# Kernel tuning notes

Hardware: AMD Instinct MI355X
Metric: run time of the kernel (lower is better)

The kernel has to match this reference:

```python
import jax, jax.numpy as jnp
import numpy as np

EPS = 1e-8

def _rasterize_mesh(face_verts, H, W):
    # face_verts: [F,3,3] = (ndc_x, ndc_y, view_z) per triangle vertex
    x0, y0, z0 = face_verts[:, 0, 0], face_verts[:, 0, 1], face_verts[:, 0, 2]
    x1, y1, z1 = face_verts[:, 1, 0], face_verts[:, 1, 1], face_verts[:, 1, 2]
    x2, y2, z2 = face_verts[:, 2, 0], face_verts[:, 2, 1], face_verts[:, 2, 2]
    area = (x1 - x0) * (y2 - y0) - (y1 - y0) * (x2 - x0)
    # cull_backfaces=True (area<=0) + degenerate + behind-camera cull
    face_ok = (area > EPS) & (z0 > 0) & (z1 > 0) & (z2 > 0)
    inv_area = jnp.where(face_ok, 1.0 / jnp.where(face_ok, area, 1.0), 0.0)
    zs = jnp.stack([z0, z1, z2], -1)  # [F,3]
    # pytorch3d NDC: +x left, +y up, pixel centers
    xs = 1.0 - (2.0 * jnp.arange(W, dtype=jnp.float32) + 1.0) / W
    ys = 1.0 - (2.0 * jnp.arange(H, dtype=jnp.float32) + 1.0) / H

    def row_fn(py):
        px = xs[:, None]  # [W,1] broadcast vs faces [F]
        w0 = ((x1 - px) * (y2 - py) - (y1 - py) * (x2 - px)) * inv_area
        w1 = ((x2 - px) * (y0 - py) - (y2 - py) * (x0 - px)) * inv_area
        w2 = ((x0 - px) * (y1 - py) - (y0 - py) * (x1 - px)) * inv_area
        inside = (w0 >= 0) & (w1 >= 0) & (w2 >= 0) & face_ok
        # perspective_correct=True: l_i = w_i * prod(other z), renormalize
        l = jnp.stack([w0 * z1 * z2, z0 * w1 * z2, z0 * z1 * w2], -1)  # [W,F,3]
        s = l.sum(-1, keepdims=True)
        b = l / jnp.where(s == 0, 1.0, s)
        # clip_barycentric_coords=True
        b = jnp.clip(b, 0.0, None)
        b = b / jnp.clip(b.sum(-1, keepdims=True), EPS, None)
        zpix = (b * zs[None]).sum(-1)  # [W,F] interpolated view-space depth
        zm = jnp.where(inside, zpix, jnp.inf)
        fidx = jnp.argmin(zm, axis=1)  # z-buffer winner per pixel
        zmin = jnp.take_along_axis(zm, fidx[:, None], 1)[:, 0]
        hit = jnp.isfinite(zmin)
        bary = jnp.take_along_axis(b, fidx[:, None, None], 1)[:, 0]  # [W,3]
        return (jnp.where(hit, fidx, -1),
                jnp.where(hit, zmin, -1.0),
                jnp.where(hit[:, None], bary, -1.0))

    return jax.lax.map(row_fn, ys)  # ([H,W],[H,W],[H,W,3])


def _forward(positions, features, faces, K, RT, H, W):
    B, V, _ = positions.shape
    Fn = faces.shape[1]
    # --- create_camera_objects: open3d/opencv KRT -> pytorch3d camera ---
    R = RT[:, :, :3]
    t = RT[:, :, 3]
    scale = min(H, W) / 2.0
    focal = jnp.stack([K[:, 0, 0], K[:, 1, 1]], -1) / scale  # [B,2] NDC focal
    p0 = -(jnp.stack([K[:, 0, 2], K[:, 1, 2]], -1)
           - jnp.array([W / 2.0, H / 2.0], jnp.float32)) / scale  # [B,2]
    sign = jnp.array([-1.0, -1.0, 1.0], jnp.float32)
    R_p = jnp.swapaxes(R, 1, 2) * sign[None, None, :]  # R^T with cols 0,1 negated
    T_p = t * sign[None, :]
    # --- _get_mesh_ndc: world -> view -> NDC (pytorch3d row-vector convention) ---
    v_view = jnp.einsum('bvi,bij->bvj', positions, R_p) + T_p[:, None, :]
    z = v_view[..., 2:3]
    xy_ndc = focal[:, None, :] * v_view[..., :2] / z + p0[:, None, :]
    verts_ndc = jnp.concatenate([xy_ndc, z], -1)  # z overwritten with view-space depth
    face_verts = jax.vmap(lambda v, f: v[f])(verts_ndc, faces)  # [B,F,3,3]
    # --- rasterize (blur_sigma=0 -> faces_per_pixel=1) ---
    p2f, zbuf, bary = jax.vmap(lambda fv: _rasterize_mesh(fv, H, W))(face_verts)
    hit = p2f >= 0
    pix_to_face = jnp.where(hit, p2f + (jnp.arange(B) * Fn)[:, None, None], -1)
    # --- interpolate_face_attributes on packed faces/verts ---
    faces_packed = (faces + (jnp.arange(B) * V)[:, None, None]).reshape(B * Fn, 3)
    feats_packed = features.reshape(B * V, -1)
    fv_idx = faces_packed[jnp.clip(pix_to_face, 0)]  # [B,H,W,3]
    attrs = feats_packed[fv_idx]                      # [B,H,W,3,C]
    pix_feats = (bary[..., None] * attrs).sum(-2)
    pix_feats = jnp.where(hit[..., None], pix_feats, 0.0)
    dists = jnp.where(hit, 0.0, -1.0)
    # add faces_per_pixel (K=1) axis, matching pytorch3d Fragments layout
    return (pix_feats[:, :, :, None, :], pix_to_face[:, :, :, None],
            zbuf[:, :, :, None], bary[:, :, :, None, :], dists[:, :, :, None])


def setup_inputs() -> dict:
    key = jax.random.key(0)
    k1, k2, k3 = jax.random.split(key, 3)
    B, V, Fn, C, H, W = 1, 8192, 16384, 64, 192, 192
    positions = jax.random.uniform(k1, (B, V, 3), jnp.float32) * 2.0 - 1.0
    features = jax.random.normal(k2, (B, V, C), jnp.float32)
    faces = jax.random.randint(k3, (B, Fn, 3), 0, V)
    K = jnp.broadcast_to(jnp.array([[180.0, 0.0, 96.0], [0.0, 180.0, 96.0],
                                    [0.0, 0.0, 1.0]], jnp.float32), (B, 3, 3))
    RT = jnp.broadcast_to(jnp.concatenate(
        [jnp.eye(3, dtype=jnp.float32),
         jnp.array([[0.0], [0.0], [3.5]], jnp.float32)], axis=1), (B, 3, 4))
    return {"positions": positions, "features": features, "faces": faces,
            "K": K, "RT": RT, "H": H, "W": W, "blur_sigma": 0}


def reference(positions, features, faces, K, RT, H, W, blur_sigma):
    # blur_sigma == 0 path of VertexShader.forward (faces_per_pixel=1)
    return _forward(positions, features, faces, K, RT, H, W)
```

## Files before the change

kernel.cpp:

```cpp
#include <hip/hip_runtime.h>
#include <stdint.h>

#define H_ 192
#define W_ 192
#define C_ 64
#define EPS_F 1e-8f
#define TILE 16
#define CHUNK 256
#define NSLICE 16

typedef unsigned long long ull;

#define OFF_FEATS 0
#define OFF_P2F   (H_*W_*C_)
#define OFF_ZBUF  (OFF_P2F + H_*W_)
#define OFF_BARY  (OFF_ZBUF + H_*W_)
#define OFF_DIST  (OFF_BARY + H_*W_*3)

__device__ __forceinline__ float xm(float a, float b){ return __fmul_rn(a,b); }
__device__ __forceinline__ float xa(float a, float b){ return __fadd_rn(a,b); }
__device__ __forceinline__ float xsb(float a, float b){ return __fsub_rn(a,b); }
__device__ __forceinline__ float xd(float a, float b){ return __fdiv_rn(a,b); }

__device__ __forceinline__ float pixcoord(int i, float dim){
    float t = xa(xm(2.0f, (float)i), 1.0f);
    return xsb(1.0f, xd(t, dim));
}

__global__ void k_init(const float* __restrict__ pos, const float* __restrict__ K,
                       const float* __restrict__ RT, float* __restrict__ verts,
                       ull* __restrict__ keys, int V){
    int i = blockIdx.x*blockDim.x + threadIdx.x;
    if (i < H_*W_) keys[i] = 0xFFFFFFFFFFFFFFFFULL;
    if (i >= V) return;
    float p0 = pos[3*i+0], p1 = pos[3*i+1], p2 = pos[3*i+2];
    const float sgn[3] = {-1.f, -1.f, 1.f};
    float vv[3];
    #pragma unroll
    for (int j=0;j<3;j++){
        float rp0 = xm(RT[j*4+0], sgn[j]);
        float rp1 = xm(RT[j*4+1], sgn[j]);
        float rp2 = xm(RT[j*4+2], sgn[j]);
        float s = xa(xa(xm(p0,rp0), xm(p1,rp1)), xm(p2,rp2));
        vv[j] = xa(s, xm(RT[j*4+3], sgn[j]));
    }
    float z = vv[2];
    const float scale = 96.0f;
    float fx = xd(K[0], scale);
    float fy = xd(K[4], scale);
    float p0x = -xd(xsb(K[2], 96.0f), scale);
    float p0y = -xd(xsb(K[5], 96.0f), scale);
    float xn = xa(xd(xm(fx, vv[0]), z), p0x);
    float yn = xa(xd(xm(fy, vv[1]), z), p0y);
    verts[4*i+0] = xn; verts[4*i+1] = yn; verts[4*i+2] = z; verts[4*i+3] = 0.f;
}

__global__ void k_faces(const int* __restrict__ faces, const float* __restrict__ verts,
                        float* __restrict__ rec, int Fn){
    int f = blockIdx.x*blockDim.x + threadIdx.x;
    if (f >= Fn) return;
    int i0 = faces[3*f+0], i1 = faces[3*f+1], i2 = faces[3*f+2];
    float x0=verts[4*i0+0], y0=verts[4*i0+1], z0=verts[4*i0+2];
    float x1=verts[4*i1+0], y1=verts[4*i1+1], z1=verts[4*i1+2];
    float x2=verts[4*i2+0], y2=verts[4*i2+1], z2=verts[4*i2+2];
    float area = xsb(xm(xsb(x1,x0), xsb(y2,y0)), xm(xsb(y1,y0), xsb(x2,x0)));
    bool ok = (area > EPS_F) && (z0 > 0.f) && (z1 > 0.f) && (z2 > 0.f);
    float inv_area = ok ? xd(1.0f, area) : 0.0f;
    float xmn, xmx, ymn, ymx, zmn;
    if (ok){
        xmn = fminf(x0, fminf(x1, x2)) - 1e-4f;
        xmx = fmaxf(x0, fmaxf(x1, x2)) + 1e-4f;
        ymn = fminf(y0, fminf(y1, y2)) - 1e-4f;
        ymx = fmaxf(y0, fmaxf(y1, y2)) + 1e-4f;
        zmn = fminf(z0, fminf(z1, z2));
    } else {
        xmn = INFINITY; xmx = -INFINITY; ymn = INFINITY; ymx = -INFINITY;
        zmn = INFINITY;
    }
    float4* q = (float4*)(rec + (size_t)f*16);
    q[0] = make_float4(x0, y0, x1, y1);
    q[1] = make_float4(x2, y2, z0, z1);
    q[2] = make_float4(z2, inv_area, zmn, 0.f);
    q[3] = make_float4(xmn, xmx, ymn, ymx);
}

__global__ __launch_bounds__(256) void k_raster(const float* __restrict__ rec,
        ull* __restrict__ keys, int Fn){
    __shared__ float lds[CHUNK*12];
    __shared__ float zl[CHUNK];
    __shared__ int   slist[CHUNK];
    __shared__ int   wcnt[4];
    int tid = threadIdx.x;
    int ix = blockIdx.x*TILE + (tid & 15);
    int iy = blockIdx.y*TILE + (tid >> 4);
    int pix = iy*W_ + ix;
    float px = pixcoord(ix, (float)W_);
    float py = pixcoord(iy, (float)H_);
    float tx_hi = pixcoord(blockIdx.x*TILE,          (float)W_);
    float tx_lo = pixcoord(blockIdx.x*TILE + TILE-1, (float)W_);
    float ty_hi = pixcoord(blockIdx.y*TILE,          (float)H_);
    float ty_lo = pixcoord(blockIdx.y*TILE + TILE-1, (float)H_);
    int perSlice = Fn / NSLICE;
    int f0 = blockIdx.z * perSlice;
    int f1 = f0 + perSlice;
    int lane = tid & 63, wv = tid >> 6;

    float zbest = INFINITY;
    int fbest = -1;

    for (int base = f0; base < f1; base += CHUNK){
        __syncthreads();
        const float4* g = (const float4*)(rec + (size_t)(base + tid)*16);
        float4 q0 = g[0], q1 = g[1], q2 = g[2], q3 = g[3];
        bool keep = (q3.x <= tx_hi) && (q3.y >= tx_lo) && (q3.z <= ty_hi) && (q3.w >= ty_lo);
        float4* l = (float4*)(lds + tid*12);
        l[0] = q0; l[1] = q1; l[2] = q2;
        ull m = __ballot(keep);
        if (lane == 0) wcnt[wv] = __popcll(m);
        __syncthreads();
        int basecnt = 0;
        #pragma unroll
        for (int w2 = 0; w2 < 4; ++w2) if (w2 < wv) basecnt += wcnt[w2];
        if (keep){
            int pos = basecnt + __popcll(m & ((1ULL << lane) - 1ULL));
            slist[pos] = tid;
            zl[pos] = q2.z;
        }
        int nsurv = wcnt[0] + wcnt[1] + wcnt[2] + wcnt[3];
        __syncthreads();

        for (int k = 0; k < nsurv; k++){
            float zminf = zl[k];
            if (!(xm(zminf, 0.999f) < zbest)) continue;
            int j = slist[k];
            const float* r = lds + j*12;
            float x0=r[0], y0=r[1], x1=r[2], y1=r[3], x2=r[4], y2=r[5];
            float dx0=xsb(x0,px), dx1=xsb(x1,px), dx2=xsb(x2,px);
            float dy0=xsb(y0,py), dy1=xsb(y1,py), dy2=xsb(y2,py);
            float e0 = xsb(xm(dx1,dy2), xm(dy1,dx2));
            float e1 = xsb(xm(dx2,dy0), xm(dy2,dx0));
            float e2 = xsb(xm(dx0,dy1), xm(dy0,dx1));
            if (e0 >= 0.f && e1 >= 0.f && e2 >= 0.f){
                float z0=r[6], z1=r[7], z2=r[8], ia=r[9];
                float w0 = xm(e0, ia), w1 = xm(e1, ia), w2 = xm(e2, ia);
                float l0 = xm(xm(w0,z1),z2);
                float l1 = xm(xm(z0,w1),z2);
                float l2 = xm(xm(z0,z1),w2);
                float s  = xa(xa(l0,l1),l2);
                float dn = (s == 0.f) ? 1.0f : s;
                float b0 = fmaxf(xd(l0,dn), 0.f);
                float b1 = fmaxf(xd(l1,dn), 0.f);
                float b2 = fmaxf(xd(l2,dn), 0.f);
                float bs = fmaxf(xa(xa(b0,b1),b2), EPS_F);
                b0 = xd(b0,bs); b1 = xd(b1,bs); b2 = xd(b2,bs);
                float zp = xa(xa(xm(b0,z0),xm(b1,z1)),xm(b2,z2));
                if (zp < zbest){ zbest = zp; fbest = base + j; }
            }
        }
    }
    if (fbest >= 0){
        ull key = (((ull)__float_as_uint(zbest)) << 32) | (unsigned)fbest;
        atomicMin(&keys[pix], key);
    }
}

__global__ __launch_bounds__(256) void k_post(const ull* __restrict__ keys,
        const float* __restrict__ rec, const float* __restrict__ feats,
        const int* __restrict__ faces, float* __restrict__ out){
    int grp = threadIdx.x >> 6;
    int c = threadIdx.x & 63;
    int pix = blockIdx.x*4 + grp;
    float* p2f  = out + OFF_P2F;
    float* zbuf = out + OFF_ZBUF;
    float* bary = out + OFF_BARY;
    float* dist = out + OFF_DIST;
    ull key = keys[pix];
    if (key == 0xFFFFFFFFFFFFFFFFULL){
        out[OFF_FEATS + pix*C_ + c] = 0.0f;
        if (c == 0){
            p2f[pix] = -1.0f; zbuf[pix] = -1.0f; dist[pix] = -1.0f;
        }
        if (c < 3) bary[3*pix+c] = -1.0f;
        return;
    }
    int f = (int)(key & 0xFFFFFFFFu);
    float z = __uint_as_float((unsigned)(key >> 32));
    int ix = pix % W_, iy = pix / W_;
    float px = pixcoord(ix, (float)W_);
    float py = pixcoord(iy, (float)H_);
    const float* r = rec + (size_t)f*16;
    float x0=r[0], y0=r[1], x1=r[2], y1=r[3], x2=r[4], y2=r[5];
    float z0=r[6], z1=r[7], z2=r[8], ia=r[9];
    float w0 = xm(xsb(xm(xsb(x1,px),xsb(y2,py)), xm(xsb(y1,py),xsb(x2,px))), ia);
    float w1 = xm(xsb(xm(xsb(x2,px),xsb(y0,py)), xm(xsb(y2,py),xsb(x0,px))), ia);
    float w2 = xm(xsb(xm(xsb(x0,px),xsb(y1,py)), xm(xsb(y0,py),xsb(x1,px))), ia);
    float l0 = xm(xm(w0,z1),z2);
    float l1 = xm(xm(z0,w1),z2);
    float l2 = xm(xm(z0,z1),w2);
    float s  = xa(xa(l0,l1),l2);
    float dn = (s == 0.f) ? 1.0f : s;
    float b0 = fmaxf(xd(l0,dn), 0.f);
    float b1 = fmaxf(xd(l1,dn), 0.f);
    float b2 = fmaxf(xd(l2,dn), 0.f);
    float bs = fmaxf(xa(xa(b0,b1),b2), EPS_F);
    b0 = xd(b0,bs); b1 = xd(b1,bs); b2 = xd(b2,bs);
    int i0 = faces[3*f+0], i1 = faces[3*f+1], i2 = faces[3*f+2];
    float res = xa(xa(xm(b0, feats[i0*C_ + c]), xm(b1, feats[i1*C_ + c])),
                   xm(b2, feats[i2*C_ + c]));
    out[OFF_FEATS + pix*C_ + c] = res;
    if (c == 0){
        p2f[pix] = (float)f; zbuf[pix] = z; dist[pix] = 0.0f;
    }
    if (c < 3){
        float bb = (c == 0) ? b0 : ((c == 1) ? b1 : b2);
        bary[3*pix+c] = bb;
    }
}

extern "C" void kernel_launch(void* const* d_in, const int* in_sizes, int n_in,
                              void* d_out, int out_size, void* d_ws, size_t ws_size,
                              hipStream_t stream) {
    const float* positions = (const float*)d_in[0];
    const float* features  = (const float*)d_in[1];
    const int*   faces     = (const int*)  d_in[2];
    const float* K         = (const float*)d_in[3];
    const float* RT        = (const float*)d_in[4];
    int V  = in_sizes[0] / 3;
    int Fn = in_sizes[2] / 3;

    float* verts = (float*)d_ws;
    float* rec   = verts + (size_t)V*4;
    ull*   keys  = (ull*)(rec + (size_t)Fn*16);

    int initN = H_*W_;
    k_init<<<(initN+255)/256, 256, 0, stream>>>(positions, K, RT, verts, keys, V);
    k_faces<<<(Fn+255)/256, 256, 0, stream>>>(faces, verts, rec, Fn);
    dim3 rg(W_/TILE, H_/TILE, NSLICE);
    k_raster<<<rg, dim3(256,1,1), 0, stream>>>(rec, keys, Fn);
    k_post<<<(H_*W_)/4, 256, 0, stream>>>(keys, rec, features, faces, (float*)d_out);
}
```

Before: 177.2 us.

## Compact visible faces, rasterize 4 rows per thread with global z-buffer early skip

Face setup now stream-compacts only valid (front-facing, in-front) faces through an atomic counter and stores the original face index, so the rasterizer loops over surviving faces only. The raster kernel uses single-wavefront 64-thread blocks, each lane covering 4 pixel rows that share x-edge terms. Slices grow to 32 with chunks of 64. Each chunk reads the global z-buffer keys to skip faces that cannot win, and partial winners are pushed with atomicMin after each chunk. The post kernel recomputes face data from the vertices, since the compacted records are no longer indexed by face id. This adds more atomics and relies on the compaction order staying consistent with the tie-break on face index.

```diff
diff --git a/kernel.cpp b/kernel.cpp
--- a/kernel.cpp
+++ b/kernel.cpp
@@ -6,8 +6,8 @@
 #define C_ 64
 #define EPS_F 1e-8f
 #define TILE 16
-#define CHUNK 256
-#define NSLICE 16
+#define CHUNK 64
+#define NSLICE 32
 
 typedef unsigned long long ull;
 
@@ -29,8 +29,9 @@
 
 __global__ void k_init(const float* __restrict__ pos, const float* __restrict__ K,
                        const float* __restrict__ RT, float* __restrict__ verts,
-                       ull* __restrict__ keys, int V){
+                       ull* __restrict__ keys, int* __restrict__ cnt, int V){
     int i = blockIdx.x*blockDim.x + threadIdx.x;
+    if (i == 0) *cnt = 0;
     if (i < H_*W_) keys[i] = 0xFFFFFFFFFFFFFFFFULL;
     if (i >= V) return;
     float p0 = pos[3*i+0], p1 = pos[3*i+1], p2 = pos[3*i+2];
@@ -56,116 +57,146 @@
 }
 
 __global__ void k_faces(const int* __restrict__ faces, const float* __restrict__ verts,
-                        float* __restrict__ rec, int Fn){
+                        float* __restrict__ rec, int* __restrict__ cnt, int Fn){
     int f = blockIdx.x*blockDim.x + threadIdx.x;
-    if (f >= Fn) return;
-    int i0 = faces[3*f+0], i1 = faces[3*f+1], i2 = faces[3*f+2];
-    float x0=verts[4*i0+0], y0=verts[4*i0+1], z0=verts[4*i0+2];
-    float x1=verts[4*i1+0], y1=verts[4*i1+1], z1=verts[4*i1+2];
-    float x2=verts[4*i2+0], y2=verts[4*i2+1], z2=verts[4*i2+2];
-    float area = xsb(xm(xsb(x1,x0), xsb(y2,y0)), xm(xsb(y1,y0), xsb(x2,x0)));
-    bool ok = (area > EPS_F) && (z0 > 0.f) && (z1 > 0.f) && (z2 > 0.f);
-    float inv_area = ok ? xd(1.0f, area) : 0.0f;
-    float xmn, xmx, ymn, ymx, zmn;
-    if (ok){
-        xmn = fminf(x0, fminf(x1, x2)) - 1e-4f;
-        xmx = fmaxf(x0, fmaxf(x1, x2)) + 1e-4f;
-        ymn = fminf(y0, fminf(y1, y2)) - 1e-4f;
-        ymx = fmaxf(y0, fmaxf(y1, y2)) + 1e-4f;
-        zmn = fminf(z0, fminf(z1, z2));
-    } else {
-        xmn = INFINITY; xmx = -INFINITY; ymn = INFINITY; ymx = -INFINITY;
-        zmn = INFINITY;
-    }
-    float4* q = (float4*)(rec + (size_t)f*16);
+    int lane = threadIdx.x & 63;
+    bool ok = false;
+    float x0=0,y0=0,z0=0,x1=0,y1=0,z1=0,x2=0,y2=0,z2=0,inv_area=0;
+    if (f < Fn){
+        int i0 = faces[3*f+0], i1 = faces[3*f+1], i2 = faces[3*f+2];
+        x0=verts[4*i0+0]; y0=verts[4*i0+1]; z0=verts[4*i0+2];
+        x1=verts[4*i1+0]; y1=verts[4*i1+1]; z1=verts[4*i1+2];
+        x2=verts[4*i2+0]; y2=verts[4*i2+1]; z2=verts[4*i2+2];
+        float area = xsb(xm(xsb(x1,x0), xsb(y2,y0)), xm(xsb(y1,y0), xsb(x2,x0)));
+        ok = (area > EPS_F) && (z0 > 0.f) && (z1 > 0.f) && (z2 > 0.f);
+        if (ok) inv_area = xd(1.0f, area);
+    }
+    ull m = __ballot(ok);
+    int nw = __popcll(m);
+    if (nw == 0) return;
+    int leader = __ffsll((long long)m) - 1;
+    int base = 0;
+    if (lane == leader) base = atomicAdd(cnt, nw);
+    base = __shfl(base, leader);
+    if (!ok) return;
+    int pos = base + __popcll(m & ((1ULL << lane) - 1ULL));
+    float xmn = fminf(x0, fminf(x1, x2)) - 1e-4f;
+    float xmx = fmaxf(x0, fmaxf(x1, x2)) + 1e-4f;
+    float ymn = fminf(y0, fminf(y1, y2)) - 1e-4f;
+    float ymx = fmaxf(y0, fmaxf(y1, y2)) + 1e-4f;
+    float zmn = fminf(z0, fminf(z1, z2));
+    float4* q = (float4*)(rec + (size_t)pos*16);
     q[0] = make_float4(x0, y0, x1, y1);
     q[1] = make_float4(x2, y2, z0, z1);
-    q[2] = make_float4(z2, inv_area, zmn, 0.f);
+    q[2] = make_float4(z2, inv_area, zmn, __int_as_float(f));
     q[3] = make_float4(xmn, xmx, ymn, ymx);
 }
 
-__global__ __launch_bounds__(256) void k_raster(const float* __restrict__ rec,
-        ull* __restrict__ keys, int Fn){
-    __shared__ float lds[CHUNK*12];
+__global__ __launch_bounds__(64) void k_raster(const float* __restrict__ rec,
+        const int* __restrict__ cnt, ull* __restrict__ keys){
+    __shared__ float lf[CHUNK*12];
     __shared__ float zl[CHUNK];
-    __shared__ int   slist[CHUNK];
-    __shared__ int   wcnt[4];
-    int tid = threadIdx.x;
-    int ix = blockIdx.x*TILE + (tid & 15);
-    int iy = blockIdx.y*TILE + (tid >> 4);
-    int pix = iy*W_ + ix;
+    __shared__ int   fi[CHUNK];
+    int lane = threadIdx.x;
+    int ix  = blockIdx.x*TILE + (lane & 15);
+    int iy0 = blockIdx.y*TILE + (lane >> 4) * 4;
     float px = pixcoord(ix, (float)W_);
-    float py = pixcoord(iy, (float)H_);
+    float py[4]; int pix[4];
+    #pragma unroll
+    for (int r=0;r<4;r++){ py[r] = pixcoord(iy0+r, (float)H_); pix[r] = (iy0+r)*W_ + ix; }
     float tx_hi = pixcoord(blockIdx.x*TILE,          (float)W_);
     float tx_lo = pixcoord(blockIdx.x*TILE + TILE-1, (float)W_);
     float ty_hi = pixcoord(blockIdx.y*TILE,          (float)H_);
     float ty_lo = pixcoord(blockIdx.y*TILE + TILE-1, (float)H_);
-    int perSlice = Fn / NSLICE;
+    int alive = *cnt;
+    int perSlice = (alive + NSLICE - 1) / NSLICE;
     int f0 = blockIdx.z * perSlice;
-    int f1 = f0 + perSlice;
-    int lane = tid & 63, wv = tid >> 6;
-
-    float zbest = INFINITY;
-    int fbest = -1;
+    int f1 = min(f0 + perSlice, alive);
+
+    float zbest[4], zskip[4]; int fbest[4], lastf[4];
+    #pragma unroll
+    for (int r=0;r<4;r++){ zbest[r]=INFINITY; zskip[r]=INFINITY; fbest[r]=-1; lastf[r]=-1; }
 
     for (int base = f0; base < f1; base += CHUNK){
+        float zmax;
+        {
+            #pragma unroll
+            for (int r=0;r<4;r++){
+                ull k = __hip_atomic_load(&keys[pix[r]], __ATOMIC_RELAXED, __HIP_MEMORY_SCOPE_AGENT);
+                float kz = __uint_as_float((unsigned)(k >> 32));
+                zskip[r] = fminf(zskip[r], kz);
+            }
+            zmax = fmaxf(fmaxf(zskip[0],zskip[1]), fmaxf(zskip[2],zskip[3]));
+        }
         __syncthreads();
-        const float4* g = (const float4*)(rec + (size_t)(base + tid)*16);
-        float4 q0 = g[0], q1 = g[1], q2 = g[2], q3 = g[3];
-        bool keep = (q3.x <= tx_hi) && (q3.y >= tx_lo) && (q3.z <= ty_hi) && (q3.w >= ty_lo);
-        float4* l = (float4*)(lds + tid*12);
-        l[0] = q0; l[1] = q1; l[2] = q2;
+        int f = base + lane;
+        bool keep = false;
+        float4 q0, q1, q2;
+        if (f < f1){
+            const float4* g = (const float4*)(rec + (size_t)f*16);
+            q0 = g[0]; q1 = g[1]; q2 = g[2];
+            float4 q3 = g[3];
+            keep = (q3.x <= tx_hi) && (q3.y >= tx_lo) && (q3.z <= ty_hi) && (q3.w >= ty_lo);
+        }
         ull m = __ballot(keep);
-        if (lane == 0) wcnt[wv] = __popcll(m);
+        int nsurv = __popcll(m);
+        if (keep){
+            int pos = __popcll(m & ((1ULL << lane) - 1ULL));
+            float4* l = (float4*)(lf + pos*12);
+            l[0] = q0; l[1] = q1; l[2] = q2;
+            zl[pos] = q2.z;
+            fi[pos] = __float_as_int(q2.w);
+        }
         __syncthreads();
-        int basecnt = 0;
+
+        for (int k = 0; k < nsurv; k++){
+            float t = xm(zl[k], 0.999f);
+            if (t >= zmax) continue;
+            const float* rr = lf + k*12;
+            float x0=rr[0], y0=rr[1], x1=rr[2], y1=rr[3], x2=rr[4], y2=rr[5];
+            float dx0=xsb(x0,px), dx1=xsb(x1,px), dx2=xsb(x2,px);
+            #pragma unroll
+            for (int r=0;r<4;r++){
+                float dy0=xsb(y0,py[r]), dy1=xsb(y1,py[r]), dy2=xsb(y2,py[r]);
+                float e0 = xsb(xm(dx1,dy2), xm(dy1,dx2));
+                float e1 = xsb(xm(dx2,dy0), xm(dy2,dx0));
+                float e2 = xsb(xm(dx0,dy1), xm(dy0,dx1));
+                if (e0 >= 0.f && e1 >= 0.f && e2 >= 0.f && t < zskip[r]){
+                    float z0=rr[6], z1=rr[7], z2=rr[8], ia=rr[9];
+                    float w0 = xm(e0, ia), w1 = xm(e1, ia), w2 = xm(e2, ia);
+                    float l0 = xm(xm(w0,z1),z2);
+                    float l1 = xm(xm(z0,w1),z2);
+                    float l2 = xm(xm(z0,z1),w2);
+                    float s  = xa(xa(l0,l1),l2);
+                    float dn = (s == 0.f) ? 1.0f : s;
+                    float b0 = fmaxf(xd(l0,dn), 0.f);
+                    float b1 = fmaxf(xd(l1,dn), 0.f);
+                    float b2 = fmaxf(xd(l2,dn), 0.f);
+                    float bs = fmaxf(xa(xa(b0,b1),b2), EPS_F);
+                    b0 = xd(b0,bs); b1 = xd(b1,bs); b2 = xd(b2,bs);
+                    float zp = xa(xa(xm(b0,z0),xm(b1,z1)),xm(b2,z2));
+                    int fidx = fi[k];
+                    if (zp < zbest[r] || (zp == zbest[r] && fidx < fbest[r])){
+                        zbest[r] = zp; fbest[r] = fidx;
+                        zskip[r] = fminf(zskip[r], zp);
+                        zmax = fmaxf(fmaxf(zskip[0],zskip[1]), fmaxf(zskip[2],zskip[3]));
+                    }
+                }
+            }
+        }
         #pragma unroll
-        for (int w2 = 0; w2 < 4; ++w2) if (w2 < wv) basecnt += wcnt[w2];
-        if (keep){
-            int pos = basecnt + __popcll(m & ((1ULL << lane) - 1ULL));
-            slist[pos] = tid;
-            zl[pos] = q2.z;
-        }
-        int nsurv = wcnt[0] + wcnt[1] + wcnt[2] + wcnt[3];
-        __syncthreads();
-
-        for (int k = 0; k < nsurv; k++){
-            float zminf = zl[k];
-            if (!(xm(zminf, 0.999f) < zbest)) continue;
-            int j = slist[k];
-            const float* r = lds + j*12;
-            float x0=r[0], y0=r[1], x1=r[2], y1=r[3], x2=r[4], y2=r[5];
-            float dx0=xsb(x0,px), dx1=xsb(x1,px), dx2=xsb(x2,px);
-            float dy0=xsb(y0,py), dy1=xsb(y1,py), dy2=xsb(y2,py);
-            float e0 = xsb(xm(dx1,dy2), xm(dy1,dx2));
-            float e1 = xsb(xm(dx2,dy0), xm(dy2,dx0));
-            float e2 = xsb(xm(dx0,dy1), xm(dy0,dx1));
-            if (e0 >= 0.f && e1 >= 0.f && e2 >= 0.f){
-                float z0=r[6], z1=r[7], z2=r[8], ia=r[9];
-                float w0 = xm(e0, ia), w1 = xm(e1, ia), w2 = xm(e2, ia);
-                float l0 = xm(xm(w0,z1),z2);
-                float l1 = xm(xm(z0,w1),z2);
-                float l2 = xm(xm(z0,z1),w2);
-                float s  = xa(xa(l0,l1),l2);
-                float dn = (s == 0.f) ? 1.0f : s;
-                float b0 = fmaxf(xd(l0,dn), 0.f);
-                float b1 = fmaxf(xd(l1,dn), 0.f);
-                float b2 = fmaxf(xd(l2,dn), 0.f);
-                float bs = fmaxf(xa(xa(b0,b1),b2), EPS_F);
-                b0 = xd(b0,bs); b1 = xd(b1,bs); b2 = xd(b2,bs);
-                float zp = xa(xa(xm(b0,z0),xm(b1,z1)),xm(b2,z2));
-                if (zp < zbest){ zbest = zp; fbest = base + j; }
+        for (int r=0;r<4;r++){
+            if (fbest[r] >= 0 && fbest[r] != lastf[r]){
+                ull key = (((ull)__float_as_uint(zbest[r])) << 32) | (unsigned)fbest[r];
+                atomicMin(&keys[pix[r]], key);
+                lastf[r] = fbest[r];
             }
         }
     }
-    if (fbest >= 0){
-        ull key = (((ull)__float_as_uint(zbest)) << 32) | (unsigned)fbest;
-        atomicMin(&keys[pix], key);
-    }
 }
 
 __global__ __launch_bounds__(256) void k_post(const ull* __restrict__ keys,
-        const float* __restrict__ rec, const float* __restrict__ feats,
+        const float* __restrict__ verts, const float* __restrict__ feats,
         const int* __restrict__ faces, float* __restrict__ out){
     int grp = threadIdx.x >> 6;
     int c = threadIdx.x & 63;
@@ -177,9 +208,7 @@
     ull key = keys[pix];
     if (key == 0xFFFFFFFFFFFFFFFFULL){
         out[OFF_FEATS + pix*C_ + c] = 0.0f;
-        if (c == 0){
-            p2f[pix] = -1.0f; zbuf[pix] = -1.0f; dist[pix] = -1.0f;
-        }
+        if (c == 0){ p2f[pix] = -1.0f; zbuf[pix] = -1.0f; dist[pix] = -1.0f; }
         if (c < 3) bary[3*pix+c] = -1.0f;
         return;
     }
@@ -188,9 +217,12 @@
     int ix = pix % W_, iy = pix / W_;
     float px = pixcoord(ix, (float)W_);
     float py = pixcoord(iy, (float)H_);
-    const float* r = rec + (size_t)f*16;
-    float x0=r[0], y0=r[1], x1=r[2], y1=r[3], x2=r[4], y2=r[5];
-    float z0=r[6], z1=r[7], z2=r[8], ia=r[9];
+    int i0 = faces[3*f+0], i1 = faces[3*f+1], i2 = faces[3*f+2];
+    float x0=verts[4*i0+0], y0=verts[4*i0+1], z0=verts[4*i0+2];
+    float x1=verts[4*i1+0], y1=verts[4*i1+1], z1=verts[4*i1+2];
+    float x2=verts[4*i2+0], y2=verts[4*i2+1], z2=verts[4*i2+2];
+    float area = xsb(xm(xsb(x1,x0), xsb(y2,y0)), xm(xsb(y1,y0), xsb(x2,x0)));
+    float ia = xd(1.0f, area);
     float w0 = xm(xsb(xm(xsb(x1,px),xsb(y2,py)), xm(xsb(y1,py),xsb(x2,px))), ia);
     float w1 = xm(xsb(xm(xsb(x2,px),xsb(y0,py)), xm(xsb(y2,py),xsb(x0,px))), ia);
     float w2 = xm(xsb(xm(xsb(x0,px),xsb(y1,py)), xm(xsb(y0,py),xsb(x1,px))), ia);
@@ -204,13 +236,10 @@
     float b2 = fmaxf(xd(l2,dn), 0.f);
     float bs = fmaxf(xa(xa(b0,b1),b2), EPS_F);
     b0 = xd(b0,bs); b1 = xd(b1,bs); b2 = xd(b2,bs);
-    int i0 = faces[3*f+0], i1 = faces[3*f+1], i2 = faces[3*f+2];
     float res = xa(xa(xm(b0, feats[i0*C_ + c]), xm(b1, feats[i1*C_ + c])),
                    xm(b2, feats[i2*C_ + c]));
     out[OFF_FEATS + pix*C_ + c] = res;
-    if (c == 0){
-        p2f[pix] = (float)f; zbuf[pix] = z; dist[pix] = 0.0f;
-    }
+    if (c == 0){ p2f[pix] = (float)f; zbuf[pix] = z; dist[pix] = 0.0f; }
     if (c < 3){
         float bb = (c == 0) ? b0 : ((c == 1) ? b1 : b2);
         bary[3*pix+c] = bb;
@@ -231,11 +260,12 @@
     float* verts = (float*)d_ws;
     float* rec   = verts + (size_t)V*4;
     ull*   keys  = (ull*)(rec + (size_t)Fn*16);
+    int*   cnt   = (int*)(keys + (size_t)H_*W_);
 
     int initN = H_*W_;
-    k_init<<<(initN+255)/256, 256, 0, stream>>>(positions, K, RT, verts, keys, V);
-    k_faces<<<(Fn+255)/256, 256, 0, stream>>>(faces, verts, rec, Fn);
+    k_init<<<(initN+255)/256, 256, 0, stream>>>(positions, K, RT, verts, keys, cnt, V);
+    k_faces<<<(Fn+255)/256, 256, 0, stream>>>(faces, verts, rec, cnt, Fn);
     dim3 rg(W_/TILE, H_/TILE, NSLICE);
-    k_raster<<<rg, dim3(256,1,1), 0, stream>>>(rec, keys, Fn);
-    k_post<<<(H_*W_)/4, 256, 0, stream>>>(keys, rec, features, faces, (float*)d_out);
-}
+    k_raster<<<rg, dim3(64,1,1), 0, stream>>>(rec, cnt, keys);
+    k_post<<<(H_*W_)/4, 256, 0, stream>>>(keys, verts, features, faces, (float*)d_out);
+}
```

New measurement: 181.2 us. 1.02x slower.

## Depth-sort faces into buckets and early-exit raster tiles via suffix z-min

Applied to the files above, without the earlier changes.

Adds a histogram/prefix/scatter pass that bins culled-in faces by minimum depth, so rasterization visits near faces first. A per-chunk suffix minimum of zmin lets each tile stop once no remaining chunk can beat the current best depth, and the grid shrinks to two slices that share progress through relaxed loads of the global key buffer. Per-pixel bbox tests and tie-breaking by face index are added, and post recomputes barycentrics from the vertices. This costs extra small launches and single-block serial kernels, and it relies on the depth distribution for the early exit to pay off.

```diff
diff --git a/kernel.cpp b/kernel.cpp
--- a/kernel.cpp
+++ b/kernel.cpp
@@ -6,8 +6,10 @@
 #define C_ 64
 #define EPS_F 1e-8f
 #define TILE 16
-#define CHUNK 256
-#define NSLICE 16
+#define RCH 256
+#define NS 2
+#define NBUCK 256
+#define MAXCH 65
 
 typedef unsigned long long ull;
 
@@ -27,10 +29,16 @@
     return xsb(1.0f, xd(t, dim));
 }
 
+__device__ __forceinline__ int zbucket(float zmn){
+    int b = (int)((zmn - 2.5f) * 128.0f);
+    return max(0, min(NBUCK-1, b));
+}
+
 __global__ void k_init(const float* __restrict__ pos, const float* __restrict__ K,
                        const float* __restrict__ RT, float* __restrict__ verts,
-                       ull* __restrict__ keys, int V){
+                       ull* __restrict__ keys, int* __restrict__ hist, int V){
     int i = blockIdx.x*blockDim.x + threadIdx.x;
+    if (i < NBUCK) hist[i] = 0;
     if (i < H_*W_) keys[i] = 0xFFFFFFFFFFFFFFFFULL;
     if (i >= V) return;
     float p0 = pos[3*i+0], p1 = pos[3*i+1], p2 = pos[3*i+2];
@@ -55,41 +63,98 @@
     verts[4*i+0] = xn; verts[4*i+1] = yn; verts[4*i+2] = z; verts[4*i+3] = 0.f;
 }
 
-__global__ void k_faces(const int* __restrict__ faces, const float* __restrict__ verts,
-                        float* __restrict__ rec, int Fn){
-    int f = blockIdx.x*blockDim.x + threadIdx.x;
+__global__ __launch_bounds__(256) void k_hist(const int* __restrict__ faces,
+        const float* __restrict__ verts, int* __restrict__ hist, int Fn){
+    __shared__ int lh[NBUCK];
+    int t = threadIdx.x;
+    lh[t] = 0;
+    __syncthreads();
+    int f = blockIdx.x*256 + t;
+    if (f < Fn){
+        int i0 = faces[3*f+0], i1 = faces[3*f+1], i2 = faces[3*f+2];
+        float4 v0 = ((const float4*)verts)[i0];
+        float4 v1 = ((const float4*)verts)[i1];
+        float4 v2 = ((const float4*)verts)[i2];
+        float area = xsb(xm(xsb(v1.x,v0.x), xsb(v2.y,v0.y)), xm(xsb(v1.y,v0.y), xsb(v2.x,v0.x)));
+        bool ok = (area > EPS_F) && (v0.z > 0.f) && (v1.z > 0.f) && (v2.z > 0.f);
+        if (ok){
+            float zmn = fminf(v0.z, fminf(v1.z, v2.z));
+            atomicAdd(&lh[zbucket(zmn)], 1);
+        }
+    }
+    __syncthreads();
+    if (lh[t]) atomicAdd(&hist[t], lh[t]);
+}
+
+__global__ __launch_bounds__(256) void k_prefix(const int* __restrict__ hist,
+        int* __restrict__ cursor, int* __restrict__ cnt){
+    __shared__ int tmp[NBUCK];
+    int t = threadIdx.x;
+    int h = hist[t];
+    tmp[t] = h;
+    __syncthreads();
+    for (int off=1; off<NBUCK; off<<=1){
+        int u = (t >= off) ? tmp[t-off] : 0;
+        __syncthreads();
+        tmp[t] += u;
+        __syncthreads();
+    }
+    cursor[t] = tmp[t] - h;
+    if (t == NBUCK-1) *cnt = tmp[NBUCK-1];
+}
+
+__global__ __launch_bounds__(256) void k_scatter(const int* __restrict__ faces,
+        const float* __restrict__ verts, int* __restrict__ cursor,
+        float* __restrict__ srec, int Fn){
+    int f = blockIdx.x*256 + threadIdx.x;
     if (f >= Fn) return;
     int i0 = faces[3*f+0], i1 = faces[3*f+1], i2 = faces[3*f+2];
-    float x0=verts[4*i0+0], y0=verts[4*i0+1], z0=verts[4*i0+2];
-    float x1=verts[4*i1+0], y1=verts[4*i1+1], z1=verts[4*i1+2];
-    float x2=verts[4*i2+0], y2=verts[4*i2+1], z2=verts[4*i2+2];
-    float area = xsb(xm(xsb(x1,x0), xsb(y2,y0)), xm(xsb(y1,y0), xsb(x2,x0)));
-    bool ok = (area > EPS_F) && (z0 > 0.f) && (z1 > 0.f) && (z2 > 0.f);
-    float inv_area = ok ? xd(1.0f, area) : 0.0f;
-    float xmn, xmx, ymn, ymx, zmn;
-    if (ok){
-        xmn = fminf(x0, fminf(x1, x2)) - 1e-4f;
-        xmx = fmaxf(x0, fmaxf(x1, x2)) + 1e-4f;
-        ymn = fminf(y0, fminf(y1, y2)) - 1e-4f;
-        ymx = fmaxf(y0, fmaxf(y1, y2)) + 1e-4f;
-        zmn = fminf(z0, fminf(z1, z2));
-    } else {
-        xmn = INFINITY; xmx = -INFINITY; ymn = INFINITY; ymx = -INFINITY;
-        zmn = INFINITY;
-    }
-    float4* q = (float4*)(rec + (size_t)f*16);
-    q[0] = make_float4(x0, y0, x1, y1);
-    q[1] = make_float4(x2, y2, z0, z1);
-    q[2] = make_float4(z2, inv_area, zmn, 0.f);
+    float4 v0 = ((const float4*)verts)[i0];
+    float4 v1 = ((const float4*)verts)[i1];
+    float4 v2 = ((const float4*)verts)[i2];
+    float area = xsb(xm(xsb(v1.x,v0.x), xsb(v2.y,v0.y)), xm(xsb(v1.y,v0.y), xsb(v2.x,v0.x)));
+    bool ok = (area > EPS_F) && (v0.z > 0.f) && (v1.z > 0.f) && (v2.z > 0.f);
+    if (!ok) return;
+    float zmn = fminf(v0.z, fminf(v1.z, v2.z));
+    int pos = atomicAdd(&cursor[zbucket(zmn)], 1);
+    float ia = xd(1.0f, area);
+    float xmn = fminf(v0.x, fminf(v1.x, v2.x)) - 1e-4f;
+    float xmx = fmaxf(v0.x, fmaxf(v1.x, v2.x)) + 1e-4f;
+    float ymn = fminf(v0.y, fminf(v1.y, v2.y)) - 1e-4f;
+    float ymx = fmaxf(v0.y, fmaxf(v1.y, v2.y)) + 1e-4f;
+    float4* q = (float4*)(srec + (size_t)pos*16);
+    q[0] = make_float4(v0.x, v0.y, v1.x, v1.y);
+    q[1] = make_float4(v2.x, v2.y, v0.z, v1.z);
+    q[2] = make_float4(v2.z, ia, zmn, __int_as_float(f));
     q[3] = make_float4(xmn, xmx, ymn, ymx);
 }
 
-__global__ __launch_bounds__(256) void k_raster(const float* __restrict__ rec,
-        ull* __restrict__ keys, int Fn){
-    __shared__ float lds[CHUNK*12];
-    __shared__ float zl[CHUNK];
-    __shared__ int   slist[CHUNK];
-    __shared__ int   wcnt[4];
+__global__ __launch_bounds__(256) void k_sufmin(const float* __restrict__ srec,
+        const int* __restrict__ cnt, float* __restrict__ sufchunk){
+    __shared__ float cm[MAXCH];
+    int t = threadIdx.x;
+    int alive = *cnt;
+    int nch = (alive + RCH-1) >> 8;
+    if (t < MAXCH){
+        float m = INFINITY;
+        if (t < nch){
+            int i0 = t << 8, i1 = min(i0 + RCH, alive);
+            for (int i = i0; i < i1; i++) m = fminf(m, srec[(size_t)i*16 + 10]);
+        }
+        cm[t] = m;
+    }
+    __syncthreads();
+    if (t == 0){
+        float run = INFINITY;
+        for (int c = MAXCH-1; c >= 0; c--){ run = fminf(run, cm[c]); sufchunk[c] = run; }
+    }
+}
+
+__global__ __launch_bounds__(256) void k_raster(const float* __restrict__ srec,
+        const int* __restrict__ cnt, const float* __restrict__ sufchunk,
+        ull* __restrict__ keys){
+    __shared__ float lf[RCH*16];
+    __shared__ int wcnt[4];
     int tid = threadIdx.x;
     int ix = blockIdx.x*TILE + (tid & 15);
     int iy = blockIdx.y*TILE + (tid >> 4);
@@ -100,72 +165,85 @@
     float tx_lo = pixcoord(blockIdx.x*TILE + TILE-1, (float)W_);
     float ty_hi = pixcoord(blockIdx.y*TILE,          (float)H_);
     float ty_lo = pixcoord(blockIdx.y*TILE + TILE-1, (float)H_);
-    int perSlice = Fn / NSLICE;
-    int f0 = blockIdx.z * perSlice;
-    int f1 = f0 + perSlice;
     int lane = tid & 63, wv = tid >> 6;
-
-    float zbest = INFINITY;
-    int fbest = -1;
-
-    for (int base = f0; base < f1; base += CHUNK){
-        __syncthreads();
-        const float4* g = (const float4*)(rec + (size_t)(base + tid)*16);
-        float4 q0 = g[0], q1 = g[1], q2 = g[2], q3 = g[3];
-        bool keep = (q3.x <= tx_hi) && (q3.y >= tx_lo) && (q3.z <= ty_hi) && (q3.w >= ty_lo);
-        float4* l = (float4*)(lds + tid*12);
-        l[0] = q0; l[1] = q1; l[2] = q2;
+    int alive = *cnt;
+    int nch = (alive + RCH-1) >> 8;
+
+    float zbest = INFINITY, zskip = INFINITY;
+    int fbest = -1, lastpub = -1;
+
+    for (int c = blockIdx.z; c < nch; c += NS){
+        ull kk = __hip_atomic_load(&keys[pix], __ATOMIC_RELAXED, __HIP_MEMORY_SCOPE_AGENT);
+        zskip = fminf(zskip, __uint_as_float((unsigned)(kk >> 32)));
+        int done = (xm(sufchunk[c], 0.999f) >= zskip) ? 1 : 0;
+        if (__syncthreads_and(done)) break;
+
+        int f = (c << 8) + tid;
+        bool keep = false;
+        float4 q0, q1, q2, q3;
+        if (f < alive){
+            const float4* g = (const float4*)(srec + (size_t)f*16);
+            q0 = g[0]; q1 = g[1]; q2 = g[2]; q3 = g[3];
+            keep = (q3.x <= tx_hi) && (q3.y >= tx_lo) && (q3.z <= ty_hi) && (q3.w >= ty_lo);
+        }
         ull m = __ballot(keep);
         if (lane == 0) wcnt[wv] = __popcll(m);
         __syncthreads();
-        int basecnt = 0;
+        int basec = 0;
         #pragma unroll
-        for (int w2 = 0; w2 < 4; ++w2) if (w2 < wv) basecnt += wcnt[w2];
+        for (int w2 = 0; w2 < 4; ++w2) if (w2 < wv) basec += wcnt[w2];
         if (keep){
-            int pos = basecnt + __popcll(m & ((1ULL << lane) - 1ULL));
-            slist[pos] = tid;
-            zl[pos] = q2.z;
+            int pos = basec + __popcll(m & ((1ULL << lane) - 1ULL));
+            float4* l = (float4*)(lf + pos*16);
+            l[0] = q0; l[1] = q1; l[2] = q2; l[3] = q3;
         }
         int nsurv = wcnt[0] + wcnt[1] + wcnt[2] + wcnt[3];
         __syncthreads();
 
         for (int k = 0; k < nsurv; k++){
-            float zminf = zl[k];
-            if (!(xm(zminf, 0.999f) < zbest)) continue;
-            int j = slist[k];
-            const float* r = lds + j*12;
-            float x0=r[0], y0=r[1], x1=r[2], y1=r[3], x2=r[4], y2=r[5];
-            float dx0=xsb(x0,px), dx1=xsb(x1,px), dx2=xsb(x2,px);
-            float dy0=xsb(y0,py), dy1=xsb(y1,py), dy2=xsb(y2,py);
-            float e0 = xsb(xm(dx1,dy2), xm(dy1,dx2));
-            float e1 = xsb(xm(dx2,dy0), xm(dy2,dx0));
-            float e2 = xsb(xm(dx0,dy1), xm(dy0,dx1));
-            if (e0 >= 0.f && e1 >= 0.f && e2 >= 0.f){
-                float z0=r[6], z1=r[7], z2=r[8], ia=r[9];
-                float w0 = xm(e0, ia), w1 = xm(e1, ia), w2 = xm(e2, ia);
-                float l0 = xm(xm(w0,z1),z2);
-                float l1 = xm(xm(z0,w1),z2);
-                float l2 = xm(xm(z0,z1),w2);
-                float s  = xa(xa(l0,l1),l2);
-                float dn = (s == 0.f) ? 1.0f : s;
-                float b0 = fmaxf(xd(l0,dn), 0.f);
-                float b1 = fmaxf(xd(l1,dn), 0.f);
-                float b2 = fmaxf(xd(l2,dn), 0.f);
-                float bs = fmaxf(xa(xa(b0,b1),b2), EPS_F);
-                b0 = xd(b0,bs); b1 = xd(b1,bs); b2 = xd(b2,bs);
-                float zp = xa(xa(xm(b0,z0),xm(b1,z1)),xm(b2,z2));
-                if (zp < zbest){ zbest = zp; fbest = base + j; }
+            const float* r = lf + k*16;
+            float t = xm(r[10], 0.999f);
+            if (t < zskip){
+                if (px >= r[12] && px <= r[13] && py >= r[14] && py <= r[15]){
+                    float x0=r[0], y0=r[1], x1=r[2], y1=r[3], x2=r[4], y2=r[5];
+                    float dx0=xsb(x0,px), dx1=xsb(x1,px), dx2=xsb(x2,px);
+                    float dy0=xsb(y0,py), dy1=xsb(y1,py), dy2=xsb(y2,py);
+                    float e0 = xsb(xm(dx1,dy2), xm(dy1,dx2));
+                    float e1 = xsb(xm(dx2,dy0), xm(dy2,dx0));
+                    float e2 = xsb(xm(dx0,dy1), xm(dy0,dx1));
+                    if (e0 >= 0.f && e1 >= 0.f && e2 >= 0.f){
+                        float z0=r[6], z1=r[7], z2=r[8], ia=r[9];
+                        float w0 = xm(e0, ia), w1 = xm(e1, ia), w2 = xm(e2, ia);
+                        float l0 = xm(xm(w0,z1),z2);
+                        float l1 = xm(xm(z0,w1),z2);
+                        float l2 = xm(xm(z0,z1),w2);
+                        float s  = xa(xa(l0,l1),l2);
+                        float dn = (s == 0.f) ? 1.0f : s;
+                        float b0 = fmaxf(xd(l0,dn), 0.f);
+                        float b1 = fmaxf(xd(l1,dn), 0.f);
+                        float b2 = fmaxf(xd(l2,dn), 0.f);
+                        float bs = fmaxf(xa(xa(b0,b1),b2), EPS_F);
+                        b0 = xd(b0,bs); b1 = xd(b1,bs); b2 = xd(b2,bs);
+                        float zp = xa(xa(xm(b0,z0),xm(b1,z1)),xm(b2,z2));
+                        int fidx = __float_as_int(r[11]);
+                        if (zp < zbest || (zp == zbest && fidx < fbest)){
+                            zbest = zp; fbest = fidx;
+                            zskip = fminf(zskip, zp);
+                        }
+                    }
+                }
             }
         }
-    }
-    if (fbest >= 0){
-        ull key = (((ull)__float_as_uint(zbest)) << 32) | (unsigned)fbest;
-        atomicMin(&keys[pix], key);
+        if (fbest >= 0 && fbest != lastpub){
+            ull key = (((ull)__float_as_uint(zbest)) << 32) | (unsigned)fbest;
+            atomicMin(&keys[pix], key);
+            lastpub = fbest;
+        }
     }
 }
 
 __global__ __launch_bounds__(256) void k_post(const ull* __restrict__ keys,
-        const float* __restrict__ rec, const float* __restrict__ feats,
+        const float* __restrict__ verts, const float* __restrict__ feats,
         const int* __restrict__ faces, float* __restrict__ out){
     int grp = threadIdx.x >> 6;
     int c = threadIdx.x & 63;
@@ -177,9 +255,7 @@
     ull key = keys[pix];
     if (key == 0xFFFFFFFFFFFFFFFFULL){
         out[OFF_FEATS + pix*C_ + c] = 0.0f;
-        if (c == 0){
-            p2f[pix] = -1.0f; zbuf[pix] = -1.0f; dist[pix] = -1.0f;
-        }
+        if (c == 0){ p2f[pix] = -1.0f; zbuf[pix] = -1.0f; dist[pix] = -1.0f; }
         if (c < 3) bary[3*pix+c] = -1.0f;
         return;
     }
@@ -188,9 +264,12 @@
     int ix = pix % W_, iy = pix / W_;
     float px = pixcoord(ix, (float)W_);
     float py = pixcoord(iy, (float)H_);
-    const float* r = rec + (size_t)f*16;
-    float x0=r[0], y0=r[1], x1=r[2], y1=r[3], x2=r[4], y2=r[5];
-    float z0=r[6], z1=r[7], z2=r[8], ia=r[9];
+    int i0 = faces[3*f+0], i1 = faces[3*f+1], i2 = faces[3*f+2];
+    float x0=verts[4*i0+0], y0=verts[4*i0+1], z0=verts[4*i0+2];
+    float x1=verts[4*i1+0], y1=verts[4*i1+1], z1=verts[4*i1+2];
+    float x2=verts[4*i2+0], y2=verts[4*i2+1], z2=verts[4*i2+2];
+    float area = xsb(xm(xsb(x1,x0), xsb(y2,y0)), xm(xsb(y1,y0), xsb(x2,x0)));
+    float ia = xd(1.0f, area);
     float w0 = xm(xsb(xm(xsb(x1,px),xsb(y2,py)), xm(xsb(y1,py),xsb(x2,px))), ia);
     float w1 = xm(xsb(xm(xsb(x2,px),xsb(y0,py)), xm(xsb(y2,py),xsb(x0,px))), ia);
     float w2 = xm(xsb(xm(xsb(x0,px),xsb(y1,py)), xm(xsb(y0,py),xsb(x1,px))), ia);
@@ -204,13 +283,10 @@
     float b2 = fmaxf(xd(l2,dn), 0.f);
     float bs = fmaxf(xa(xa(b0,b1),b2), EPS_F);
     b0 = xd(b0,bs); b1 = xd(b1,bs); b2 = xd(b2,bs);
-    int i0 = faces[3*f+0], i1 = faces[3*f+1], i2 = faces[3*f+2];
     float res = xa(xa(xm(b0, feats[i0*C_ + c]), xm(b1, feats[i1*C_ + c])),
                    xm(b2, feats[i2*C_ + c]));
     out[OFF_FEATS + pix*C_ + c] = res;
-    if (c == 0){
-        p2f[pix] = (float)f; zbuf[pix] = z; dist[pix] = 0.0f;
-    }
+    if (c == 0){ p2f[pix] = (float)f; zbuf[pix] = z; dist[pix] = 0.0f; }
     if (c < 3){
         float bb = (c == 0) ? b0 : ((c == 1) ? b1 : b2);
         bary[3*pix+c] = bb;
@@ -228,14 +304,21 @@
     int V  = in_sizes[0] / 3;
     int Fn = in_sizes[2] / 3;
 
-    float* verts = (float*)d_ws;
-    float* rec   = verts + (size_t)V*4;
-    ull*   keys  = (ull*)(rec + (size_t)Fn*16);
+    float* verts    = (float*)d_ws;
+    float* srec     = verts + (size_t)V*4;
+    ull*   keys     = (ull*)(srec + (size_t)Fn*16);
+    int*   cnt      = (int*)(keys + (size_t)H_*W_);
+    int*   hist     = cnt + 1;
+    int*   cursor   = hist + NBUCK;
+    float* sufchunk = (float*)(cursor + NBUCK);
 
     int initN = H_*W_;
-    k_init<<<(initN+255)/256, 256, 0, stream>>>(positions, K, RT, verts, keys, V);
-    k_faces<<<(Fn+255)/256, 256, 0, stream>>>(faces, verts, rec, Fn);
-    dim3 rg(W_/TILE, H_/TILE, NSLICE);
-    k_raster<<<rg, dim3(256,1,1), 0, stream>>>(rec, keys, Fn);
-    k_post<<<(H_*W_)/4, 256, 0, stream>>>(keys, rec, features, faces, (float*)d_out);
-}
+    k_init   <<<(initN+255)/256, 256, 0, stream>>>(positions, K, RT, verts, keys, hist, V);
+    k_hist   <<<(Fn+255)/256, 256, 0, stream>>>(faces, verts, hist, Fn);
+    k_prefix <<<1, 256, 0, stream>>>(hist, cursor, cnt);
+    k_scatter<<<(Fn+255)/256, 256, 0, stream>>>(faces, verts, cursor, srec, Fn);
+    k_sufmin <<<1, 256, 0, stream>>>(srec, cnt, sufchunk);
+    dim3 rg(W_/TILE, H_/TILE, NS);
+    k_raster <<<rg, 256, 0, stream>>>(srec, cnt, sufchunk, keys);
+    k_post   <<<(H_*W_)/4, 256, 0, stream>>>(keys, verts, features, faces, (float*)d_out);
+}
```

Result: slower. 410.9 us (+131.8%).
